# Kernel optimization log

Measured on AMD Instinct MI355X. Metric: run time of the kernel, lower is better.

Reference implementation:

```python
import jax, jax.numpy as jnp
import numpy as np

D_MODEL = 1024
N_HEADS = 8
D_KEYS = D_MODEL // N_HEADS  # 128
D_LLM = 4096


def setup_inputs() -> dict:
    key = jax.random.key(0)
    ks = jax.random.split(key, 11)
    Bm, Lq, Vs = 8, 1024, 2048
    inner = D_KEYS * N_HEADS  # 1024
    s = 0.02
    return {
        "Q": jax.random.normal(ks[0], (Bm, Lq, D_MODEL), jnp.float32),
        "K_src": jax.random.normal(ks[1], (Vs, D_LLM), jnp.float32),
        "V_src": jax.random.normal(ks[2], (Vs, D_LLM), jnp.float32),
        "Wq": jax.random.normal(ks[3], (D_MODEL, inner), jnp.float32) * s,
        "bq": jnp.zeros((inner,), jnp.float32),
        "Wk": jax.random.normal(ks[4], (D_LLM, inner), jnp.float32) * s,
        "bk": jnp.zeros((inner,), jnp.float32),
        "Wv": jax.random.normal(ks[5], (D_LLM, inner), jnp.float32) * s,
        "bv": jnp.zeros((inner,), jnp.float32),
        "Wo": jax.random.normal(ks[6], (inner, D_LLM), jnp.float32) * s,
        "bo": jnp.zeros((D_LLM,), jnp.float32),
    }


def reference(Q, K_src, V_src, Wq, bq, Wk, bk, Wv, bv, Wo, bo):
    Bm, Lq, _ = Q.shape
    Vs, d_llm = K_src.shape
    H = N_HEADS
    Ek = d_llm // H  # NOTE: torch code scales by d_llm//H, not d_keys
    q = (Q @ Wq + bq).reshape(Bm, Lq, H, -1)           # [B,Lq,H,E]
    k = (K_src @ Wk + bk).reshape(Vs, H, -1)            # [S,H,E]
    v = (V_src @ Wv + bv).reshape(Vs, H, -1)            # [S,H,E]
    scale = 1.0 / jnp.sqrt(jnp.asarray(Ek, q.dtype))
    scores = jnp.einsum("blhe,she->bhls", q, k)         # [B,H,Lq,S]
    A = jax.nn.softmax(scale * scores, axis=-1)         # dropout = identity (eval)
    out = jnp.einsum("bhls,she->blhe", A, v)            # [B,Lq,H,E]
    out = out.reshape(Bm, Lq, -1)
    return out @ Wo + bo                                 # [B,Lq,d_llm]
```

## Files before the change

kernel.cpp:

```cpp
#include <hip/hip_runtime.h>
#include <hip/hip_bf16.h>


typedef __bf16 bf16x8 __attribute__((ext_vector_type(8)));
typedef float  f32x4  __attribute__((ext_vector_type(4)));

union V16 { uint4 u; bf16x8 v; };
__device__ __forceinline__ bf16x8 ld16v(const void* p) {
  V16 t; t.u = *(const uint4*)p; return t.v;
}
__device__ __forceinline__ uint4 pack8(float4 a, float4 b) {
  V16 t;
  t.v[0] = (__bf16)a.x; t.v[1] = (__bf16)a.y; t.v[2] = (__bf16)a.z; t.v[3] = (__bf16)a.w;
  t.v[4] = (__bf16)b.x; t.v[5] = (__bf16)b.y; t.v[6] = (__bf16)b.z; t.v[7] = (__bf16)b.w;
  return t.u;
}
__device__ __forceinline__ void dma16(const void* g, void* l) {
  __builtin_amdgcn_global_load_lds(
      (const __attribute__((address_space(1))) unsigned int*)g,
      (__attribute__((address_space(3))) unsigned int*)l, 16, 0, 0);
}
__device__ __forceinline__ int chunk_of(int row, int gc) {
  return row * 4 + (gc ^ ((row >> 1) & 3));
}

__global__ __launch_bounds__(256) void transpose_k(const float* __restrict__ W,
                                                   __bf16* __restrict__ Wt, int K, int N,
                                                   float scale) {
  __shared__ __bf16 t[32][33];
  int tx = threadIdx.x & 31, ty = threadIdx.x >> 5;
  int n0 = blockIdx.x * 32, k0 = blockIdx.y * 32;
#pragma unroll
  for (int r = 0; r < 32; r += 8)
    t[ty + r][tx] = (__bf16)(W[(size_t)(k0 + ty + r) * N + n0 + tx] * scale);
  __syncthreads();
#pragma unroll
  for (int r = 0; r < 32; r += 8) Wt[(size_t)(n0 + ty + r) * K + k0 + tx] = t[tx][ty + r];
}

template <typename AT, typename CT>
__device__ __forceinline__ void gemm_core(__bf16* As, __bf16* Bs,
                                          const AT* __restrict__ A,
                                          const __bf16* __restrict__ Bt,
                                          const float* __restrict__ bias,
                                          CT* __restrict__ C,
                                          int M, int N, int K, int lda, int trans,
                                          int m0, int n0, float bscale) {
  const int tid = threadIdx.x;
  const int lane = tid & 63, wave = tid >> 6;
  const int g = lane >> 4, l16 = lane & 15;
  const int wr = wave >> 1, wc = wave & 1;
  int aoff[4], boff[4];
#pragma unroll
  for (int mf = 0; mf < 4; mf++) aoff[mf] = chunk_of(wr * 64 + mf * 16 + l16, g) * 8;
#pragma unroll
  for (int nf = 0; nf < 4; nf++) boff[nf] = chunk_of(wc * 64 + nf * 16 + l16, g) * 8;

  f32x4 acc[4][4] = {};
  for (int k0 = 0; k0 < K; k0 += 32) {
    __syncthreads();
    if constexpr (sizeof(AT) == 2) {
#pragma unroll
      for (int rnd = 0; rnd < 2; rnd++) {
        int cstart = wave * 128 + rnd * 64;
        int p = cstart + lane;
        int row = p >> 2, gc = (p & 3) ^ ((row >> 1) & 3);
        dma16((const __bf16*)A + (size_t)(m0 + row) * lda + k0 + gc * 8,
              As + (size_t)cstart * 8);
      }
    } else {
#pragma unroll
      for (int i = 0; i < 2; i++) {
        int p = tid + i * 256;
        int row = p >> 2, gc = (p & 3) ^ ((row >> 1) & 3);
        const float* ap = (const float*)A + (size_t)(m0 + row) * lda + k0 + gc * 8;
        float4 f0 = *(const float4*)ap;
        float4 f1 = *(const float4*)(ap + 4);
        *(uint4*)(As + p * 8) = pack8(f0, f1);
      }
    }
#pragma unroll
    for (int rnd = 0; rnd < 2; rnd++) {
      int cstart = wave * 128 + rnd * 64;
      int p = cstart + lane;
      int row = p >> 2, gc = (p & 3) ^ ((row >> 1) & 3);
      dma16(Bt + (size_t)(n0 + row) * (size_t)K + k0 + gc * 8,
            Bs + (size_t)cstart * 8);
    }
    __syncthreads();
    bf16x8 af[4], bff[4];
#pragma unroll
    for (int mf = 0; mf < 4; mf++) af[mf]  = ld16v(As + aoff[mf]);
#pragma unroll
    for (int nf = 0; nf < 4; nf++) bff[nf] = ld16v(Bs + boff[nf]);
#pragma unroll
    for (int mf = 0; mf < 4; mf++)
#pragma unroll
      for (int nf = 0; nf < 4; nf++)
        acc[mf][nf] = __builtin_amdgcn_mfma_f32_16x16x32_bf16(af[mf], bff[nf], acc[mf][nf], 0, 0, 0);
  }
#pragma unroll
  for (int nf = 0; nf < 4; nf++) {
    int col = n0 + wc * 64 + nf * 16 + l16;
    float bv = bias[col] * bscale;
#pragma unroll
    for (int mf = 0; mf < 4; mf++) {
      int rowb = m0 + wr * 64 + mf * 16 + g * 4;
      if constexpr (sizeof(CT) == 2) {
        if (trans) {
          union { __bf16 h[4]; uint2 u; } pk;
#pragma unroll
          for (int r = 0; r < 4; r++) pk.h[r] = (__bf16)(acc[mf][nf][r] + bv);
          *(uint2*)&((__bf16*)C)[(size_t)col * M + rowb] = pk.u;
        } else {
#pragma unroll
          for (int r = 0; r < 4; r++)
            ((__bf16*)C)[(size_t)(rowb + r) * N + col] = (__bf16)(acc[mf][nf][r] + bv);
        }
      } else {
#pragma unroll
        for (int r = 0; r < 4; r++)
          ((float*)C)[(size_t)(rowb + r) * N + col] = acc[mf][nf][r] + bv;
      }
    }
  }
}

__global__ __launch_bounds__(256) void gemm_f_b(const float* __restrict__ A,
                                                const __bf16* __restrict__ Bt,
                                                const float* __restrict__ bias,
                                                __bf16* __restrict__ C,
                                                int M, int N, int K, int lda, int trans,
                                                float bscale) {
  __shared__ __align__(16) __bf16 As[128 * 32];
  __shared__ __align__(16) __bf16 Bs[128 * 32];
  gemm_core<float, __bf16>(As, Bs, A, Bt, bias, C, M, N, K, lda, trans,
                           blockIdx.x * 128, blockIdx.y * 128, bscale);
}

__global__ __launch_bounds__(256) void gemm_b_f(const __bf16* __restrict__ A,
                                                const __bf16* __restrict__ Bt,
                                                const float* __restrict__ bias,
                                                float* __restrict__ C,
                                                int M, int N, int K, int lda, int trans) {
  __shared__ __align__(16) __bf16 As[128 * 32];
  __shared__ __align__(16) __bf16 Bs[128 * 32];
  gemm_core<__bf16, float>(As, Bs, A, Bt, bias, C, M, N, K, lda, trans,
                           blockIdx.x * 128, blockIdx.y * 128, 1.0f);
}

__global__ __launch_bounds__(256) void gemm_kv(const float* __restrict__ A0, const __bf16* __restrict__ B0t,
                                               const float* __restrict__ b0, __bf16* __restrict__ C0,
                                               const float* __restrict__ A1, const __bf16* __restrict__ B1t,
                                               const float* __restrict__ b1, __bf16* __restrict__ C1) {
  __shared__ __align__(16) __bf16 As[128 * 32];
  __shared__ __align__(16) __bf16 Bs[128 * 32];
  if (blockIdx.z == 0)
    gemm_core<float, __bf16>(As, Bs, A0, B0t, b0, C0, 2048, 1024, 4096, 4096, 0,
                             blockIdx.x * 128, blockIdx.y * 128, 1.0f);
  else
    gemm_core<float, __bf16>(As, Bs, A1, B1t, b1, C1, 2048, 1024, 4096, 4096, 1,
                             blockIdx.x * 128, blockIdx.y * 128, 1.0f);
}

__global__ __launch_bounds__(256, 4) void attn_k(const __bf16* __restrict__ q,
                                                 const __bf16* __restrict__ k,
                                                 const __bf16* __restrict__ vt,
                                                 __bf16* __restrict__ o) {
  __shared__ __align__(16) union {
    __bf16 ks[64 * 128];
    __bf16 ps[64 * 72];
  } u;
  __shared__ __align__(16) __bf16 vs[128 * 64];
  const int tid = threadIdx.x, lane = tid & 63, wave = tid >> 6;
  const int g = lane >> 4, l16 = lane & 15;
  const int h = blockIdx.y, q0 = blockIdx.x * 64;

  bf16x8 qf[4];
#pragma unroll
  for (int kk = 0; kk < 4; kk++)
    qf[kk] = ld16v(q + (size_t)(q0 + wave * 16 + l16) * 1024 + h * 128 + kk * 32 + g * 8);

  f32x4 accO[8] = {};
  float m_i[4], l_i[4];
#pragma unroll
  for (int r = 0; r < 4; r++) { m_i[r] = -1e30f; l_i[r] = 0.f; }

  for (int s0 = 0; s0 < 2048; s0 += 64) {
    __syncthreads();
#pragma unroll
    for (int i = 0; i < 4; i++) {
      int c = wave * 256 + i * 64 + lane;
      int row = c >> 4, gc = (c & 15) ^ (row & 7);
      dma16(k + (size_t)(s0 + row) * 1024 + h * 128 + gc * 8,
            u.ks + (wave * 256 + i * 64) * 8);
    }
#pragma unroll
    for (int i = 0; i < 4; i++) {
      int c = wave * 256 + i * 64 + lane;
      int row = c >> 3, cc = (c & 7) ^ (row & 7);
      dma16(vt + (size_t)(h * 128 + row) * 2048 + s0 + cc * 8,
            vs + (wave * 256 + i * 64) * 8);
    }
    __syncthreads();

    f32x4 sc[4] = {};
    __builtin_amdgcn_s_setprio(1);
#pragma unroll
    for (int kk = 0; kk < 4; kk++) {
      bf16x8 kf[4];
#pragma unroll
      for (int nf = 0; nf < 4; nf++) {
        int row = nf * 16 + l16;
        kf[nf] = ld16v(u.ks + (row * 16 + ((kk * 4 + g) ^ (row & 7))) * 8);
      }
#pragma unroll
      for (int nf = 0; nf < 4; nf++)
        sc[nf] = __builtin_amdgcn_mfma_f32_16x16x32_bf16(qf[kk], kf[nf], sc[nf], 0, 0, 0);
    }
    __builtin_amdgcn_s_setprio(0);

#pragma unroll
    for (int r = 0; r < 4; r++) {
      float mx = fmaxf(fmaxf(sc[0][r], sc[1][r]), fmaxf(sc[2][r], sc[3][r]));
#pragma unroll
      for (int off = 1; off < 16; off <<= 1) mx = fmaxf(mx, __shfl_xor(mx, off));
      float mn = fmaxf(m_i[r], mx);
      float alpha = exp2f(m_i[r] - mn);
      float rs = 0.f;
#pragma unroll
      for (int nf = 0; nf < 4; nf++) {
        float p = exp2f(sc[nf][r] - mn);
        sc[nf][r] = p;
        rs += p;
      }
#pragma unroll
      for (int off = 1; off < 16; off <<= 1) rs += __shfl_xor(rs, off);
      m_i[r] = mn;
      l_i[r] = l_i[r] * alpha + rs;
#pragma unroll
      for (int ef = 0; ef < 8; ef++) accO[ef][r] *= alpha;
    }

    __syncthreads();

#pragma unroll
    for (int nf = 0; nf < 4; nf++)
#pragma unroll
      for (int r = 0; r < 4; r++) {
        int prow = wave * 16 + g * 4 + r;
        u.ps[prow * 72 + nf * 16 + l16] = (__bf16)sc[nf][r];
      }

    __builtin_amdgcn_s_setprio(1);
#pragma unroll
    for (int kk = 0; kk < 2; kk++) {
      bf16x8 pf = ld16v(u.ps + (wave * 16 + l16) * 72 + kk * 32 + g * 8);
#pragma unroll
      for (int ef = 0; ef < 8; ef++) {
        int vrow = ef * 16 + l16;
        bf16x8 vf = ld16v(vs + (vrow * 8 + ((kk * 4 + g) ^ (vrow & 7))) * 8);
        accO[ef] = __builtin_amdgcn_mfma_f32_16x16x32_bf16(pf, vf, accO[ef], 0, 0, 0);
      }
    }
    __builtin_amdgcn_s_setprio(0);
  }

  float inv[4];
#pragma unroll
  for (int r = 0; r < 4; r++) inv[r] = 1.0f / l_i[r];
#pragma unroll
  for (int ef = 0; ef < 8; ef++)
#pragma unroll
    for (int r = 0; r < 4; r++) {
      int row = q0 + wave * 16 + g * 4 + r;
      o[(size_t)row * 1024 + h * 128 + ef * 16 + l16] = (__bf16)(accO[ef][r] * inv[r]);
    }
}

extern "C" void kernel_launch(void* const* d_in, const int* in_sizes, int n_in,
                              void* d_out, int out_size, void* d_ws, size_t ws_size,
                              hipStream_t stream) {
  const float* Q   = (const float*)d_in[0];
  const float* Ksr = (const float*)d_in[1];
  const float* Vsr = (const float*)d_in[2];
  const float* Wq  = (const float*)d_in[3];
  const float* bq  = (const float*)d_in[4];
  const float* Wk  = (const float*)d_in[5];
  const float* bk  = (const float*)d_in[6];
  const float* Wv  = (const float*)d_in[7];
  const float* bv  = (const float*)d_in[8];
  const float* Wo  = (const float*)d_in[9];
  const float* bo  = (const float*)d_in[10];
  __bf16* ws = (__bf16*)d_ws;
  const size_t MB = 1024 * 1024;
  __bf16* qb  = ws;
  __bf16* kb  = ws + 8  * MB;
  __bf16* vtb = ws + 10 * MB;
  __bf16* at  = ws + 12 * MB;
  __bf16* WqT = ws + 20 * MB;
  __bf16* WkT = ws + 21 * MB;
  __bf16* WvT = ws + 25 * MB;
  __bf16* WoT = ws + 29 * MB;

  const float qscale = 0.044194173824159216f * 1.4426950408889634f;

  transpose_k<<<dim3(32, 32),  256, 0, stream>>>(Wq, WqT, 1024, 1024, qscale);
  transpose_k<<<dim3(32, 128), 256, 0, stream>>>(Wk, WkT, 4096, 1024, 1.0f);
  transpose_k<<<dim3(32, 128), 256, 0, stream>>>(Wv, WvT, 4096, 1024, 1.0f);
  transpose_k<<<dim3(128, 32), 256, 0, stream>>>(Wo, WoT, 1024, 4096, 1.0f);

  gemm_f_b<<<dim3(64, 8), 256, 0, stream>>>(Q, WqT, bq, qb, 8192, 1024, 1024, 1024, 0, qscale);
  gemm_kv<<<dim3(16, 8, 2), 256, 0, stream>>>(Ksr, WkT, bk, kb, Vsr, WvT, bv, vtb);
  attn_k<<<dim3(128, 8), 256, 0, stream>>>(qb, kb, vtb, at);
  gemm_b_f<<<dim3(64, 32), 256, 0, stream>>>(at, WoT, bo, (float*)d_out, 8192, 4096, 1024, 1024, 0);
}
```

Baseline: 682.9 us.

## Double-buffer K/V tiles in attention with 8-wave blocks and fast exp2

The attention kernel now uses 512 threads per block covering 128 query rows, sharing each K/V tile across twice as many waves. K and V tiles are double-buffered in LDS, and the next tile is prefetched with global_load_lds while the current one is computed, using explicit waitcnt and barriers. The P scratch buffer gets its own XOR-swizzled layout, which removes a barrier. exp2f is replaced by raw v_exp_f32 inline asm. The larger LDS footprint (about 80KB) and bigger blocks may lower occupancy, and the hand-written waitcnt counts have to match the number of outstanding DMA loads exactly.

```diff
diff --git a/kernel.cpp b/kernel.cpp
--- a/kernel.cpp
+++ b/kernel.cpp
@@ -19,6 +19,11 @@
   __builtin_amdgcn_global_load_lds(
       (const __attribute__((address_space(1))) unsigned int*)g,
       (__attribute__((address_space(3))) unsigned int*)l, 16, 0, 0);
+}
+__device__ __forceinline__ float exp2_fast(float x) {
+  float r;
+  asm("v_exp_f32 %0, %1\n\ts_nop 1" : "=v"(r) : "v"(x));
+  return r;
 }
 __device__ __forceinline__ int chunk_of(int row, int gc) {
   return row * 4 + (gc ^ ((row >> 1) & 3));
@@ -163,18 +168,19 @@
                              blockIdx.x * 128, blockIdx.y * 128, 1.0f);
 }
 
-__global__ __launch_bounds__(256, 4) void attn_k(const __bf16* __restrict__ q,
+__global__ __launch_bounds__(512, 4) void attn_k(const __bf16* __restrict__ q,
                                                  const __bf16* __restrict__ k,
                                                  const __bf16* __restrict__ vt,
                                                  __bf16* __restrict__ o) {
-  __shared__ __align__(16) union {
-    __bf16 ks[64 * 128];
-    __bf16 ps[64 * 72];
-  } u;
-  __shared__ __align__(16) __bf16 vs[128 * 64];
+  __shared__ __align__(16) __bf16 ks[2][64 * 128];
+  __shared__ __align__(16) __bf16 vs[2][128 * 64];
+  __shared__ __align__(16) __bf16 ps[128 * 64];
   const int tid = threadIdx.x, lane = tid & 63, wave = tid >> 6;
   const int g = lane >> 4, l16 = lane & 15;
-  const int h = blockIdx.y, q0 = blockIdx.x * 64;
+  const int h = blockIdx.y, q0 = blockIdx.x * 128;
+
+  const __bf16* kbase = k + (size_t)h * 128;
+  const __bf16* vbase = vt + (size_t)(h * 128) * 2048;
 
   bf16x8 qf[4];
 #pragma unroll
@@ -186,23 +192,46 @@
 #pragma unroll
   for (int r = 0; r < 4; r++) { m_i[r] = -1e30f; l_i[r] = 0.f; }
 
-  for (int s0 = 0; s0 < 2048; s0 += 64) {
-    __syncthreads();
-#pragma unroll
-    for (int i = 0; i < 4; i++) {
-      int c = wave * 256 + i * 64 + lane;
+  {
+#pragma unroll
+    for (int i = 0; i < 2; i++) {
+      int c = wave * 128 + i * 64 + lane;
       int row = c >> 4, gc = (c & 15) ^ (row & 7);
-      dma16(k + (size_t)(s0 + row) * 1024 + h * 128 + gc * 8,
-            u.ks + (wave * 256 + i * 64) * 8);
-    }
-#pragma unroll
-    for (int i = 0; i < 4; i++) {
-      int c = wave * 256 + i * 64 + lane;
+      dma16(kbase + (size_t)row * 1024 + gc * 8, &ks[0][(wave * 128 + i * 64) * 8]);
+    }
+#pragma unroll
+    for (int i = 0; i < 2; i++) {
+      int c = wave * 128 + i * 64 + lane;
       int row = c >> 3, cc = (c & 7) ^ (row & 7);
-      dma16(vt + (size_t)(h * 128 + row) * 2048 + s0 + cc * 8,
-            vs + (wave * 256 + i * 64) * 8);
-    }
-    __syncthreads();
+      dma16(vbase + (size_t)row * 2048 + cc * 8, &vs[0][(wave * 128 + i * 64) * 8]);
+    }
+  }
+
+  for (int t = 0; t < 32; t++) {
+    const int cur = t & 1;
+    asm volatile("s_waitcnt lgkmcnt(0)" ::: "memory");
+    __builtin_amdgcn_s_barrier();
+    __builtin_amdgcn_sched_barrier(0);
+    {
+      const int sn = ((t + 1) & 31) * 64;
+#pragma unroll
+      for (int i = 0; i < 2; i++) {
+        int c = wave * 128 + i * 64 + lane;
+        int row = c >> 4, gc = (c & 15) ^ (row & 7);
+        dma16(kbase + (size_t)(sn + row) * 1024 + gc * 8,
+              &ks[cur ^ 1][(wave * 128 + i * 64) * 8]);
+      }
+#pragma unroll
+      for (int i = 0; i < 2; i++) {
+        int c = wave * 128 + i * 64 + lane;
+        int row = c >> 3, cc = (c & 7) ^ (row & 7);
+        dma16(vbase + (size_t)row * 2048 + sn + cc * 8,
+              &vs[cur ^ 1][(wave * 128 + i * 64) * 8]);
+      }
+    }
+    asm volatile("s_waitcnt vmcnt(4)" ::: "memory");
+    __builtin_amdgcn_s_barrier();
+    __builtin_amdgcn_sched_barrier(0);
 
     f32x4 sc[4] = {};
     __builtin_amdgcn_s_setprio(1);
@@ -212,7 +241,7 @@
 #pragma unroll
       for (int nf = 0; nf < 4; nf++) {
         int row = nf * 16 + l16;
-        kf[nf] = ld16v(u.ks + (row * 16 + ((kk * 4 + g) ^ (row & 7))) * 8);
+        kf[nf] = ld16v(&ks[cur][(row * 16 + ((kk * 4 + g) ^ (row & 7))) * 8]);
       }
 #pragma unroll
       for (int nf = 0; nf < 4; nf++)
@@ -226,11 +255,11 @@
 #pragma unroll
       for (int off = 1; off < 16; off <<= 1) mx = fmaxf(mx, __shfl_xor(mx, off));
       float mn = fmaxf(m_i[r], mx);
-      float alpha = exp2f(m_i[r] - mn);
+      float alpha = exp2_fast(m_i[r] - mn);
       float rs = 0.f;
 #pragma unroll
       for (int nf = 0; nf < 4; nf++) {
-        float p = exp2f(sc[nf][r] - mn);
+        float p = exp2_fast(sc[nf][r] - mn);
         sc[nf][r] = p;
         rs += p;
       }
@@ -242,24 +271,24 @@
       for (int ef = 0; ef < 8; ef++) accO[ef][r] *= alpha;
     }
 
-    __syncthreads();
-
 #pragma unroll
     for (int nf = 0; nf < 4; nf++)
 #pragma unroll
       for (int r = 0; r < 4; r++) {
         int prow = wave * 16 + g * 4 + r;
-        u.ps[prow * 72 + nf * 16 + l16] = (__bf16)sc[nf][r];
+        int cc = nf * 2 + (l16 >> 3);
+        ps[(prow * 8 + (cc ^ (prow & 7))) * 8 + (l16 & 7)] = (__bf16)sc[nf][r];
       }
 
     __builtin_amdgcn_s_setprio(1);
 #pragma unroll
     for (int kk = 0; kk < 2; kk++) {
-      bf16x8 pf = ld16v(u.ps + (wave * 16 + l16) * 72 + kk * 32 + g * 8);
+      int prow = wave * 16 + l16;
+      bf16x8 pf = ld16v(&ps[(prow * 8 + ((kk * 4 + g) ^ (prow & 7))) * 8]);
 #pragma unroll
       for (int ef = 0; ef < 8; ef++) {
         int vrow = ef * 16 + l16;
-        bf16x8 vf = ld16v(vs + (vrow * 8 + ((kk * 4 + g) ^ (vrow & 7))) * 8);
+        bf16x8 vf = ld16v(&vs[cur][(vrow * 8 + ((kk * 4 + g) ^ (vrow & 7))) * 8]);
         accO[ef] = __builtin_amdgcn_mfma_f32_16x16x32_bf16(pf, vf, accO[ef], 0, 0, 0);
       }
     }
@@ -312,6 +341,6 @@
 
   gemm_f_b<<<dim3(64, 8), 256, 0, stream>>>(Q, WqT, bq, qb, 8192, 1024, 1024, 1024, 0, qscale);
   gemm_kv<<<dim3(16, 8, 2), 256, 0, stream>>>(Ksr, WkT, bk, kb, Vsr, WvT, bv, vtb);
-  attn_k<<<dim3(128, 8), 256, 0, stream>>>(qb, kb, vtb, at);
+  attn_k<<<dim3(64, 8), 512, 0, stream>>>(qb, kb, vtb, at);
   gemm_b_f<<<dim3(64, 32), 256, 0, stream>>>(at, WoT, bo, (float*)d_out, 8192, 4096, 1024, 1024, 0);
 }
```

Result: faster. 658.7 us (-3.5%).
